# Optimization experiments

Measured on AMD Instinct MI355X. Metric: run time of the kernel, lower is better.

Reference implementation:

```python
import jax, jax.numpy as jnp
import numpy as np

B, L, F, P = 128, 256, 4, 4   # dialogs, dialog length, future/past links
IN, H, C = 1024, 256, 7
N = B * L


def _build_edges():
    # same structure as build_intra_graph: self-loop + F future + P past per node
    i = np.arange(L)
    ss, tt = [], []
    for d in range(-P, F + 1):
        j = i + d
        m = (j >= 0) & (j < L)
        ss.append(i[m]); tt.append(j[m])
    s = np.concatenate(ss); t = np.concatenate(tt)
    offs = (np.arange(B) * L)[:, None]
    S = (s[None, :] + offs).ravel()
    T = (t[None, :] + offs).ravel()
    return np.stack([S, T]).astype(np.int32)


def setup_inputs() -> dict:
    key = jax.random.key(0)
    ks = jax.random.split(key, 16)
    ei = _build_edges()
    speakers = np.asarray(jax.random.randint(ks[0], (N,), 0, 2), dtype=np.int32)
    rel = (speakers[ei[0]] * speakers[ei[1]]).astype(np.int32)
    sd_in = 1.0 / np.sqrt(IN)
    sd_h = 1.0 / np.sqrt(H)
    return {
        "input": jax.random.normal(ks[1], (N, IN), jnp.float32),
        "dialog_lengths": jnp.full((B,), L, jnp.int32),
        "speakers": jnp.asarray(speakers),
        "labels": jax.random.randint(ks[2], (N,), 0, C, jnp.int32),
        "edge_index": jnp.asarray(ei),
        "rel_type": jnp.asarray(rel),
        # RGCNConv(IN, H, num_relations=2): per-relation weight, root weight, bias
        "W_rgcn": jax.random.normal(ks[3], (2, IN, H), jnp.float32) * sd_in,
        "W_root": jax.random.normal(ks[4], (IN, H), jnp.float32) * sd_in,
        "b_rgcn": jax.random.normal(ks[5], (H,), jnp.float32) * 0.01,
        # GraphConv(H, H): lin_rel (on aggregated neighbors, with bias), lin_root (no bias)
        "W_rel": jax.random.normal(ks[6], (H, H), jnp.float32) * sd_h,
        "b_rel": jax.random.normal(ks[7], (H,), jnp.float32) * 0.01,
        "W_grt": jax.random.normal(ks[8], (H, H), jnp.float32) * sd_h,
        # skip_con: Linear(IN, H)
        "W_skip": jax.random.normal(ks[9], (IN, H), jnp.float32) * sd_in,
        "b_skip": jax.random.normal(ks[10], (H,), jnp.float32) * 0.01,
        # classify: Linear(H, C)
        "W_cls": jax.random.normal(ks[11], (H, C), jnp.float32) * sd_h,
        "b_cls": jax.random.normal(ks[12], (C,), jnp.float32) * 0.01,
    }


def reference(input, dialog_lengths, speakers, labels, edge_index, rel_type,
              W_rgcn, W_root, b_rgcn, W_rel, b_rel, W_grt,
              W_skip, b_skip, W_cls, b_cls):
    n = input.shape[0]
    src, dst = edge_index[0], edge_index[1]
    seg = jax.ops.segment_sum

    # --- RGCNConv: out_i = x_i @ W_root + b + sum_r mean_{j in N_r(i)} x_j @ W_r
    t = jnp.einsum('ni,rio->rno', input, W_rgcn)      # [2, N, H]
    msg = t[rel_type, src]                            # [E, H] relation-specific messages
    h = input @ W_root + b_rgcn
    for r in range(2):
        m = (rel_type == r).astype(input.dtype)       # [E]
        s = seg(msg * m[:, None], dst, num_segments=n)
        cnt = seg(m, dst, num_segments=n)
        h = h + s / jnp.maximum(cnt, 1.0)[:, None]    # mean aggregation per relation

    # --- GraphConv (aggr='add'): out_i = W_rel @ sum_j h_j + b_rel + W_grt @ h_i
    neigh = seg(h[src], dst, num_segments=n)          # [N, H]
    h2 = neigh @ W_rel + b_rel + h @ W_grt

    # --- skip connection + classifier
    out = (h2 + input @ W_skip + b_skip) @ W_cls + b_cls  # [N, C]

    # --- cross entropy (mean)
    logp = jax.nn.log_softmax(out, axis=-1)
    loss = -jnp.mean(jnp.take_along_axis(logp, labels[:, None].astype(jnp.int32), axis=1))
    return out, loss
```

## Files before the change

### kernel.cpp

```cpp
#include <hip/hip_runtime.h>

#define NN 32768
#define INF 1024
#define HF 256

typedef __bf16 bf16x8 __attribute__((ext_vector_type(8)));
typedef float f32x4 __attribute__((ext_vector_type(4)));
typedef unsigned short u16x8 __attribute__((ext_vector_type(8)));

__device__ __forceinline__ float bf2f(unsigned short u) {
  union { unsigned int i; float f; } v; v.i = ((unsigned int)u) << 16; return v.f;
}
__device__ __forceinline__ unsigned short f2bf(float f) {
  union { float f; unsigned int i; } v; v.f = f;
  unsigned int x = v.i;
  return (unsigned short)((x + 0x7fffu + ((x >> 16) & 1u)) >> 16);
}

__device__ __forceinline__ void ld_lds16(const unsigned short* g, unsigned short* l) {
  __builtin_amdgcn_global_load_lds(
      (__attribute__((address_space(1))) const unsigned int*)g,
      (__attribute__((address_space(3))) unsigned int*)l, 16, 0, 0);
}

__global__ __launch_bounds__(256)
void diagcn_prep(const float* __restrict__ x, const float* __restrict__ Wrgcn,
                 const float* __restrict__ Wroot, const float* __restrict__ Wskip,
                 const float* __restrict__ Wgrt, const float* __restrict__ Wrel,
                 unsigned short* __restrict__ Xbf, unsigned short* __restrict__ WbigT,
                 unsigned short* __restrict__ WsmT, float* __restrict__ loss) {
  int bid = blockIdx.x;
  if (bid < 32768) {
    if (bid == 0 && threadIdx.x == 0) loss[0] = 0.f;
    int idx = bid * 256 + threadIdx.x;
    float4 v = ((const float4*)x)[idx];
    ushort4 u; u.x = f2bf(v.x); u.y = f2bf(v.y); u.z = f2bf(v.z); u.w = f2bf(v.w);
    ((ushort4*)Xbf)[idx] = u;
    return;
  }
  __shared__ float tile[64 * 65];
  int tb = bid - 32768;
  const float* src;
  int k0, ncol0;
  unsigned short* dst;
  int ldd, nrow0;
  if (tb < 256) {
    int tn = tb >> 4, tk = tb & 15;
    int mat = tn >> 2;
    src = (mat == 0) ? Wrgcn : (mat == 1) ? (Wrgcn + 262144) : (mat == 2) ? Wroot : Wskip;
    k0 = tk * 64; ncol0 = (tn & 3) * 64;
    dst = WbigT; ldd = 1024; nrow0 = tn * 64;
  } else {
    int t2 = tb - 256;
    int tn = t2 >> 3, tk = t2 & 7;
    src = (tk < 4) ? Wgrt : Wrel;
    k0 = (tk & 3) * 64; ncol0 = tn * 64;
    dst = WsmT; ldd = 512; nrow0 = tn * 64;
  }
  int kdst0 = (tb < 256) ? k0 : (((tb - 256) & 7) * 64);
  int c = threadIdx.x & 63, rb = threadIdx.x >> 6;
#pragma unroll
  for (int it = 0; it < 16; ++it) {
    int r = rb + it * 4;
    tile[r * 65 + c] = src[(size_t)(k0 + r) * 256 + ncol0 + c];
  }
  __syncthreads();
  int kk = threadIdx.x & 63;
#pragma unroll
  for (int it = 0; it < 16; ++it) {
    int nn = rb + it * 4;
    dst[(size_t)(nrow0 + nn) * ldd + kdst0 + kk] = f2bf(tile[kk * 65 + nn]);
  }
}

template<bool STG, int VM, bool LAST>
__device__ __forceinline__ void g1_tile(int t,
    const unsigned short* __restrict__ gA0, const unsigned short* __restrict__ gB0,
    unsigned short* SH, int w, int abase, int bbase, int sw8,
    bf16x8 (&av)[4], bf16x8 (&bv)[4], bf16x8 (&nav)[4], bf16x8 (&nbv)[4],
    f32x4 (&acc)[8][4]) {
  unsigned short* Ab = SH + ((t & 3) << 14);
  unsigned short* Bb = Ab + 8192;
  bf16x8 av2[4];
#pragma unroll
  for (int i = 0; i < 4; ++i)
    av2[i] = *(const bf16x8*)&Ab[(abase + 64 + i * 16) * 32 + sw8];
  __builtin_amdgcn_sched_barrier(0);
  if (STG) {
    unsigned short* dA = SH + (((t + 3) & 3) << 14) + (w << 10);
    const unsigned short* gA = gA0 + (t + 3) * 32;
    ld_lds16(gA, dA);
    ld_lds16(gA + 16 * 1024, dA + 512);
    unsigned short* dB = SH + (((t + 3) & 3) << 14) + 8192 + (w << 10);
    const unsigned short* gB = gB0 + (t + 3) * 32;
    ld_lds16(gB, dB);
    ld_lds16(gB + 16 * 1024, dB + 512);
  }
  asm volatile("s_waitcnt lgkmcnt(4)");
  __builtin_amdgcn_sched_barrier(0);
  __builtin_amdgcn_s_setprio(1);
#pragma unroll
  for (int i = 0; i < 4; ++i)
#pragma unroll
    for (int j = 0; j < 4; ++j)
      acc[i][j] = __builtin_amdgcn_mfma_f32_16x16x32_bf16(av[i], bv[j], acc[i][j], 0, 0, 0);
  __builtin_amdgcn_s_setprio(0);
  __builtin_amdgcn_sched_barrier(0);
  if constexpr (VM == 8) asm volatile("s_waitcnt vmcnt(8)" ::: "memory");
  else if constexpr (VM == 4) asm volatile("s_waitcnt vmcnt(4)" ::: "memory");
  else if constexpr (VM == 0) asm volatile("s_waitcnt vmcnt(0)" ::: "memory");
  __builtin_amdgcn_s_barrier();
  if constexpr (!LAST) {
    unsigned short* An = SH + (((t + 1) & 3) << 14);
    unsigned short* Bn = An + 8192;
#pragma unroll
    for (int i = 0; i < 4; ++i)
      nav[i] = *(const bf16x8*)&An[(abase + i * 16) * 32 + sw8];
    __builtin_amdgcn_sched_barrier(0);
    asm volatile("s_waitcnt lgkmcnt(4)");
    __builtin_amdgcn_sched_barrier(0);
    __builtin_amdgcn_s_setprio(1);
#pragma unroll
    for (int i = 0; i < 2; ++i)
#pragma unroll
      for (int j = 0; j < 4; ++j)
        acc[4 + i][j] = __builtin_amdgcn_mfma_f32_16x16x32_bf16(av2[i], bv[j], acc[4 + i][j], 0, 0, 0);
    __builtin_amdgcn_s_setprio(0);
    __builtin_amdgcn_sched_barrier(0);
#pragma unroll
    for (int j = 0; j < 4; ++j)
      nbv[j] = *(const bf16x8*)&Bn[(bbase + j * 16) * 32 + sw8];
    __builtin_amdgcn_sched_barrier(0);
    __builtin_amdgcn_s_setprio(1);
#pragma unroll
    for (int i = 2; i < 4; ++i)
#pragma unroll
      for (int j = 0; j < 4; ++j)
        acc[4 + i][j] = __builtin_amdgcn_mfma_f32_16x16x32_bf16(av2[i], bv[j], acc[4 + i][j], 0, 0, 0);
    __builtin_amdgcn_s_setprio(0);
    __builtin_amdgcn_s_barrier();
  } else {
    asm volatile("s_waitcnt lgkmcnt(0)");
    __builtin_amdgcn_sched_barrier(0);
#pragma unroll
    for (int i = 0; i < 4; ++i)
#pragma unroll
      for (int j = 0; j < 4; ++j)
        acc[4 + i][j] = __builtin_amdgcn_mfma_f32_16x16x32_bf16(av2[i], bv[j], acc[4 + i][j], 0, 0, 0);
  }
}

__global__ __launch_bounds__(512, 2)
void diagcn_gemm1(const unsigned short* __restrict__ A, const unsigned short* __restrict__ BT,
                  unsigned short* __restrict__ Y) {
  __shared__ unsigned short SH[65536];
  const int tid = threadIdx.x;
  const int w = tid >> 6, lane = tid & 63;
  const int quad = lane >> 4, l15 = lane & 15;
  const int wm = w >> 2, wn = w & 3;
  const int b = blockIdx.x;
  const int wg = ((b & 7) << 6) + (b >> 3);
  const int m0 = (wg >> 2) << 8;
  const int n0 = (wg & 3) << 8;
  const int abase = wm * 128 + l15;
  const int bbase = wn * 64 + l15;
  const int sw8 = ((quad ^ ((l15 >> 1) & 3)) << 3);
  const int csrc8 = (((lane & 3) ^ ((lane >> 3) & 3)) << 3);
  const unsigned short* gA0 = A + (size_t)(m0 + w * 32 + (lane >> 2)) * 1024 + csrc8;
  const unsigned short* gB0 = BT + (size_t)(n0 + w * 32 + (lane >> 2)) * 1024 + csrc8;

  f32x4 acc[8][4] = {};
  bf16x8 avA[4], bvA[4], avB[4], bvB[4];

#pragma unroll
  for (int tt = 0; tt < 3; ++tt) {
    unsigned short* dA = SH + (tt << 14) + (w << 10);
    ld_lds16(gA0 + tt * 32, dA);
    ld_lds16(gA0 + tt * 32 + 16 * 1024, dA + 512);
    unsigned short* dB = SH + (tt << 14) + 8192 + (w << 10);
    ld_lds16(gB0 + tt * 32, dB);
    ld_lds16(gB0 + tt * 32 + 16 * 1024, dB + 512);
  }
  asm volatile("s_waitcnt vmcnt(8)" ::: "memory");
  __builtin_amdgcn_s_barrier();
#pragma unroll
  for (int i = 0; i < 4; ++i)
    avA[i] = *(const bf16x8*)&SH[(abase + i * 16) * 32 + sw8];
#pragma unroll
  for (int j = 0; j < 4; ++j)
    bvA[j] = *(const bf16x8*)&SH[8192 + (bbase + j * 16) * 32 + sw8];
  __builtin_amdgcn_sched_barrier(0);

#pragma unroll 1
  for (int tt = 0; tt < 14; ++tt) {
    g1_tile<true, 8, false>(2 * tt, gA0, gB0, SH, w, abase, bbase, sw8,
                            avA, bvA, avB, bvB, acc);
    g1_tile<true, 8, false>(2 * tt + 1, gA0, gB0, SH, w, abase, bbase, sw8,
                            avB, bvB, avA, bvA, acc);
  }
  g1_tile<true, 8, false>(28, gA0, gB0, SH, w, abase, bbase, sw8, avA, bvA, avB, bvB, acc);
  g1_tile<false, 4, false>(29, gA0, gB0, SH, w, abase, bbase, sw8, avB, bvB, avA, bvA, acc);
  g1_tile<false, 0, false>(30, gA0, gB0, SH, w, abase, bbase, sw8, avA, bvA, avB, bvB, acc);
  g1_tile<false, -1, true>(31, gA0, gB0, SH, w, abase, bbase, sw8, avB, bvB, avA, bvA, acc);

#pragma unroll
  for (int i = 0; i < 8; ++i)
#pragma unroll
    for (int j = 0; j < 4; ++j) {
      const int row = m0 + wm * 128 + i * 16 + quad * 4;
      const int col = n0 + wn * 64 + j * 16 + l15;
#pragma unroll
      for (int r = 0; r < 4; ++r)
        Y[(size_t)(row + r) * 1024 + col] = f2bf(acc[i][j][r]);
    }
}

__global__ __launch_bounds__(256)
void diagcn_h(const unsigned short* __restrict__ Y, const int* __restrict__ spk,
              const float* __restrict__ brgcn, unsigned short* __restrict__ A2) {
  int b = blockIdx.x;
  int wv = threadIdx.x >> 6, lane = threadIdx.x & 63;
  int half = lane >> 5, li = lane & 31, c0 = li << 3;
  int node = ((b & 7) << 12) + ((b >> 3) << 3) + wv * 2 + half;
  int p = node & 255, dbase = node - p;
  int si = spk[node];
  float a0[8] = {}, a1[8] = {};
  float n0 = 0.f, n1 = 0.f;
#pragma unroll
  for (int d = -4; d <= 4; ++d) {
    int pj = p + d;
    float w = (pj >= 0 && pj < 256) ? 1.f : 0.f;
    int jc = pj < 0 ? 0 : (pj > 255 ? 255 : pj);
    int nj = dbase + jc;
    int rel = si & spk[nj];
    u16x8 v = *(const u16x8*)&Y[(size_t)nj * 1024 + (rel << 8) + c0];
    float w1 = rel ? w : 0.f, w0 = rel ? 0.f : w;
#pragma unroll
    for (int k = 0; k < 8; ++k) {
      float f = bf2f(v[k]);
      a0[k] += f * w0; a1[k] += f * w1;
    }
    n0 += w0; n1 += w1;
  }
  u16x8 vr = *(const u16x8*)&Y[(size_t)node * 1024 + 512 + c0];
  float i0 = 1.f / fmaxf(n0, 1.f), i1 = 1.f / fmaxf(n1, 1.f);
  u16x8 u;
#pragma unroll
  for (int k = 0; k < 8; ++k)
    u[k] = f2bf(bf2f(vr[k]) + brgcn[c0 + k] + a0[k] * i0 + a1[k] * i1);
  *(u16x8*)&A2[(size_t)node * 512 + c0] = u;
}

__global__ __launch_bounds__(256)
void diagcn_neigh(unsigned short* __restrict__ A2) {
  int b = blockIdx.x;
  int wv = threadIdx.x >> 6, lane = threadIdx.x & 63;
  int half = lane >> 5, li = lane & 31, c0 = li << 3;
  int node = ((b & 7) << 12) + ((b >> 3) << 3) + wv * 2 + half;
  int p = node & 255, dbase = node - p;
  float s[8] = {};
#pragma unroll
  for (int d = -4; d <= 4; ++d) {
    int pj = p + d;
    float w = (pj >= 0 && pj < 256) ? 1.f : 0.f;
    int jc = pj < 0 ? 0 : (pj > 255 ? 255 : pj);
    u16x8 v = *(const u16x8*)&A2[(size_t)(dbase + jc) * 512 + c0];
#pragma unroll
    for (int k = 0; k < 8; ++k) s[k] += bf2f(v[k]) * w;
  }
  u16x8 u;
#pragma unroll
  for (int k = 0; k < 8; ++k) u[k] = f2bf(s[k]);
  *(u16x8*)&A2[(size_t)node * 512 + 256 + c0] = u;
}

__global__ __launch_bounds__(256)
void diagcn_gemm2(const unsigned short* __restrict__ A, const unsigned short* __restrict__ BT,
                  const unsigned short* __restrict__ Y, const float* __restrict__ Wcls,
                  const float* __restrict__ bcls, const float* __restrict__ brel,
                  const float* __restrict__ bskip, const int* __restrict__ labels,
                  float* __restrict__ out, float* __restrict__ loss) {
  const int K = 512;
  __shared__ unsigned short As[64 * 64];
  __shared__ unsigned short Bs[256 * 64];
  __shared__ float Wc[2312];
  for (int i = threadIdx.x; i < 2312; i += 256) {
    float v;
    if (i < 1792) v = Wcls[i];
    else if (i < 1799) v = bcls[i - 1792];
    else if (i < 1800) v = 0.f;
    else if (i < 2056) v = brel[i - 1800];
    else v = bskip[i - 2056];
    Wc[i] = v;
  }
  const int tid = threadIdx.x;
  const int w = tid >> 6, lane = tid & 63;
  const int quad = lane >> 4, l15 = lane & 15;
  const int b = blockIdx.x;
  const int m0 = (((b & 7) << 6) + (b >> 3)) << 6;
  const int rowg = lane >> 3;
  const int kbsw = (lane & 7) ^ rowg;

  f32x4 acc[16] = {};
  const unsigned short* Abase = A + (size_t)m0 * K + kbsw * 8;
  const unsigned short* Bbase = BT + kbsw * 8;

  for (int k0 = 0; k0 < K; k0 += 64) {
#pragma unroll
    for (int t = 0; t < 2; ++t) {
      int grp = w * 2 + t;
      ld_lds16(Abase + (size_t)(grp * 8 + rowg) * K + k0, &As[grp * 512]);
    }
#pragma unroll
    for (int t = 0; t < 8; ++t) {
      int grp = w * 8 + t;
      ld_lds16(Bbase + (size_t)(grp * 8 + rowg) * K + k0, &Bs[grp * 512]);
    }
    __syncthreads();
#pragma unroll
    for (int ks = 0; ks < 2; ++ks) {
      int kb = ks * 4 + quad;
      int ra = w * 16 + l15;
      bf16x8 av = *(const bf16x8*)&As[ra * 64 + ((kb ^ (ra & 7)) << 3)];
#pragma unroll
      for (int j = 0; j < 16; ++j) {
        int rb2 = j * 16 + l15;
        bf16x8 bv = *(const bf16x8*)&Bs[rb2 * 64 + ((kb ^ (rb2 & 7)) << 3)];
        acc[j] = __builtin_amdgcn_mfma_f32_16x16x32_bf16(av, bv, acc[j], 0, 0, 0);
      }
    }
    __syncthreads();
  }

  float wsum[4][7] = {};
#pragma unroll
  for (int j = 0; j < 16; ++j) {
    int col = j * 16 + l15;
    float bb = Wc[1800 + col] + Wc[2056 + col];
#pragma unroll
    for (int r = 0; r < 4; ++r) {
      int row = m0 + w * 16 + quad * 4 + r;
      float z = acc[j][r] + bb + bf2f(Y[(size_t)row * 1024 + 768 + col]);
#pragma unroll
      for (int c = 0; c < 7; ++c) wsum[r][c] += z * Wc[col * 7 + c];
    }
  }
#pragma unroll
  for (int o = 1; o < 16; o <<= 1)
#pragma unroll
    for (int r = 0; r < 4; ++r)
#pragma unroll
      for (int c = 0; c < 7; ++c) wsum[r][c] += __shfl_xor(wsum[r][c], o, 64);

  float lsum = 0.f;
#pragma unroll
  for (int r = 0; r < 4; ++r) {
    int row = m0 + w * 16 + quad * 4 + r;
    float o7[7], mx = -1e30f;
#pragma unroll
    for (int c = 0; c < 7; ++c) {
      o7[c] = wsum[r][c] + Wc[1792 + c];
      mx = fmaxf(mx, o7[c]);
    }
    if (l15 < 7) out[(size_t)row * 7 + l15] = o7[l15];
    float s = 0.f;
#pragma unroll
    for (int c = 0; c < 7; ++c) s += expf(o7[c] - mx);
    int lab = labels[row];
    lsum += mx + logf(s) - o7[lab];
  }
  lsum += __shfl_xor(lsum, 16, 64);
  lsum += __shfl_xor(lsum, 32, 64);
  if (lane == 0) atomicAdd(loss, lsum * (1.0f / (float)NN));
}

extern "C" void kernel_launch(void* const* d_in, const int* in_sizes, int n_in,
                              void* d_out, int out_size, void* d_ws, size_t ws_size,
                              hipStream_t stream) {
  const float* x      = (const float*)d_in[0];
  const int* speakers = (const int*)d_in[2];
  const int* labels   = (const int*)d_in[3];
  const float* Wrgcn  = (const float*)d_in[6];
  const float* Wroot  = (const float*)d_in[7];
  const float* brgcn  = (const float*)d_in[8];
  const float* Wrel   = (const float*)d_in[9];
  const float* brel   = (const float*)d_in[10];
  const float* Wgrt   = (const float*)d_in[11];
  const float* Wskip  = (const float*)d_in[12];
  const float* bskip  = (const float*)d_in[13];
  const float* Wcls   = (const float*)d_in[14];
  const float* bcls   = (const float*)d_in[15];
  float* out = (float*)d_out;
  float* loss = out + (size_t)NN * 7;

  const size_t OFF_XBF  = 0;
  const size_t OFF_WBIG = 67108864;
  const size_t OFF_WSM  = 69206016;
  const size_t OFF_Y    = 69468160;
  const size_t OFF_A2   = 136577024;
  const size_t NEED     = 170131456;
  if (ws_size < NEED) return;

  char* ws = (char*)d_ws;
  unsigned short* Xbf   = (unsigned short*)(ws + OFF_XBF);
  unsigned short* WbigT = (unsigned short*)(ws + OFF_WBIG);
  unsigned short* WsmT  = (unsigned short*)(ws + OFF_WSM);
  unsigned short* Y     = (unsigned short*)(ws + OFF_Y);
  unsigned short* A2    = (unsigned short*)(ws + OFF_A2);

  diagcn_prep<<<dim3(33056), dim3(256), 0, stream>>>(x, Wrgcn, Wroot, Wskip, Wgrt, Wrel,
                                                     Xbf, WbigT, WsmT, loss);
  diagcn_gemm1<<<dim3(512), dim3(512), 0, stream>>>(Xbf, WbigT, Y);
  diagcn_h<<<dim3(NN / 8), dim3(256), 0, stream>>>(Y, speakers, brgcn, A2);
  diagcn_neigh<<<dim3(NN / 8), dim3(256), 0, stream>>>(A2);
  diagcn_gemm2<<<dim3(512), dim3(256), 0, stream>>>(A2, WsmT, Y, Wcls, bcls, brel, bskip,
                                                    labels, out, loss);
}
```

Baseline: 366.6 us.

## Fuse RGCN aggregation and neighbor sum into one kernel via LDS halo

Merges the h-computation and neighbor-sum kernels into one kernel that processes 64 nodes per block. Each block computes h for its nodes plus a 4-node halo on each side into shared memory, writes h to A2, then sums the 9-node neighborhoods from LDS. This removes a kernel launch and the re-read of A2 from global memory, at the cost of recomputing the 8 halo rows per block and using fewer, larger blocks (512 instead of 4096).

```diff
diff --git a/kernel.cpp b/kernel.cpp
--- a/kernel.cpp
+++ b/kernel.cpp
@@ -216,62 +216,73 @@
 }
 
 __global__ __launch_bounds__(256)
-void diagcn_h(const unsigned short* __restrict__ Y, const int* __restrict__ spk,
-              const float* __restrict__ brgcn, unsigned short* __restrict__ A2) {
+void diagcn_hn(const unsigned short* __restrict__ Y, const int* __restrict__ spk,
+               const float* __restrict__ brgcn, unsigned short* __restrict__ A2) {
+  __shared__ unsigned short hbuf[72 * 256];
   int b = blockIdx.x;
+  int node0 = ((b & 7) << 12) + ((b >> 3) << 6);
+  int d0 = node0 & ~255;
   int wv = threadIdx.x >> 6, lane = threadIdx.x & 63;
   int half = lane >> 5, li = lane & 31, c0 = li << 3;
-  int node = ((b & 7) << 12) + ((b >> 3) << 3) + wv * 2 + half;
-  int p = node & 255, dbase = node - p;
-  int si = spk[node];
-  float a0[8] = {}, a1[8] = {};
-  float n0 = 0.f, n1 = 0.f;
-#pragma unroll
-  for (int d = -4; d <= 4; ++d) {
-    int pj = p + d;
-    float w = (pj >= 0 && pj < 256) ? 1.f : 0.f;
-    int jc = pj < 0 ? 0 : (pj > 255 ? 255 : pj);
-    int nj = dbase + jc;
-    int rel = si & spk[nj];
-    u16x8 v = *(const u16x8*)&Y[(size_t)nj * 1024 + (rel << 8) + c0];
-    float w1 = rel ? w : 0.f, w0 = rel ? 0.f : w;
-#pragma unroll
-    for (int k = 0; k < 8; ++k) {
-      float f = bf2f(v[k]);
-      a0[k] += f * w0; a1[k] += f * w1;
-    }
-    n0 += w0; n1 += w1;
-  }
-  u16x8 vr = *(const u16x8*)&Y[(size_t)node * 1024 + 512 + c0];
-  float i0 = 1.f / fmaxf(n0, 1.f), i1 = 1.f / fmaxf(n1, 1.f);
-  u16x8 u;
-#pragma unroll
-  for (int k = 0; k < 8; ++k)
-    u[k] = f2bf(bf2f(vr[k]) + brgcn[c0 + k] + a0[k] * i0 + a1[k] * i1);
-  *(u16x8*)&A2[(size_t)node * 512 + c0] = u;
-}
-
-__global__ __launch_bounds__(256)
-void diagcn_neigh(unsigned short* __restrict__ A2) {
-  int b = blockIdx.x;
-  int wv = threadIdx.x >> 6, lane = threadIdx.x & 63;
-  int half = lane >> 5, li = lane & 31, c0 = li << 3;
-  int node = ((b & 7) << 12) + ((b >> 3) << 3) + wv * 2 + half;
-  int p = node & 255, dbase = node - p;
-  float s[8] = {};
-#pragma unroll
-  for (int d = -4; d <= 4; ++d) {
-    int pj = p + d;
-    float w = (pj >= 0 && pj < 256) ? 1.f : 0.f;
-    int jc = pj < 0 ? 0 : (pj > 255 ? 255 : pj);
-    u16x8 v = *(const u16x8*)&A2[(size_t)(dbase + jc) * 512 + c0];
-#pragma unroll
-    for (int k = 0; k < 8; ++k) s[k] += bf2f(v[k]) * w;
-  }
-  u16x8 u;
-#pragma unroll
-  for (int k = 0; k < 8; ++k) u[k] = f2bf(s[k]);
-  *(u16x8*)&A2[(size_t)node * 512 + 256 + c0] = u;
+  int slot = wv * 2 + half;
+
+#pragma unroll 1
+  for (int pass = 0; pass < 9; ++pass) {
+    int idx = pass * 8 + slot;
+    int src = node0 - 4 + idx;
+    int sc = src < d0 ? d0 : (src > d0 + 255 ? d0 + 255 : src);
+    int p = sc & 255;
+    int si = spk[sc];
+    float a0[8] = {}, a1[8] = {};
+    float n0 = 0.f, n1 = 0.f;
+#pragma unroll
+    for (int d = -4; d <= 4; ++d) {
+      int pj = p + d;
+      float w = (pj >= 0 && pj < 256) ? 1.f : 0.f;
+      int jc = pj < 0 ? 0 : (pj > 255 ? 255 : pj);
+      int nj = d0 + jc;
+      int rel = si & spk[nj];
+      u16x8 v = *(const u16x8*)&Y[(size_t)nj * 1024 + (rel << 8) + c0];
+      float w1 = rel ? w : 0.f, w0 = rel ? 0.f : w;
+#pragma unroll
+      for (int k = 0; k < 8; ++k) {
+        float f = bf2f(v[k]);
+        a0[k] += f * w0; a1[k] += f * w1;
+      }
+      n0 += w0; n1 += w1;
+    }
+    u16x8 vr = *(const u16x8*)&Y[(size_t)sc * 1024 + 512 + c0];
+    float i0 = 1.f / fmaxf(n0, 1.f), i1 = 1.f / fmaxf(n1, 1.f);
+    u16x8 u;
+#pragma unroll
+    for (int k = 0; k < 8; ++k)
+      u[k] = f2bf(bf2f(vr[k]) + brgcn[c0 + k] + a0[k] * i0 + a1[k] * i1);
+    *(u16x8*)&hbuf[idx * 256 + c0] = u;
+    if (idx >= 4 && idx < 68)
+      *(u16x8*)&A2[(size_t)(node0 + idx - 4) * 512 + c0] = u;
+  }
+  __syncthreads();
+
+#pragma unroll 1
+  for (int pass = 0; pass < 8; ++pass) {
+    int idx = pass * 8 + slot;
+    int node = node0 + idx;
+    int p = node & 255;
+    float s[8] = {};
+#pragma unroll
+    for (int d = -4; d <= 4; ++d) {
+      int pj = p + d;
+      float w = (pj >= 0 && pj < 256) ? 1.f : 0.f;
+      int lidx = idx + 4 + d;
+      u16x8 v = *(const u16x8*)&hbuf[lidx * 256 + c0];
+#pragma unroll
+      for (int k = 0; k < 8; ++k) s[k] += bf2f(v[k]) * w;
+    }
+    u16x8 u;
+#pragma unroll
+    for (int k = 0; k < 8; ++k) u[k] = f2bf(s[k]);
+    *(u16x8*)&A2[(size_t)node * 512 + 256 + c0] = u;
+  }
 }
 
 __global__ __launch_bounds__(256)
@@ -411,8 +422,7 @@
   diagcn_prep<<<dim3(33056), dim3(256), 0, stream>>>(x, Wrgcn, Wroot, Wskip, Wgrt, Wrel,
                                                      Xbf, WbigT, WsmT, loss);
   diagcn_gemm1<<<dim3(512), dim3(512), 0, stream>>>(Xbf, WbigT, Y);
-  diagcn_h<<<dim3(NN / 8), dim3(256), 0, stream>>>(Y, speakers, brgcn, A2);
-  diagcn_neigh<<<dim3(NN / 8), dim3(256), 0, stream>>>(A2);
+  diagcn_hn<<<dim3(512), dim3(256), 0, stream>>>(Y, speakers, brgcn, A2);
   diagcn_gemm2<<<dim3(512), dim3(256), 0, stream>>>(A2, WsmT, Y, Wcls, bcls, brel, bskip,
                                                     labels, out, loss);
 }
```

After: 369.1 us. No clear change (+0.7%).
